# Performance work log

Measured on AMD Instinct MI355X. Metric: run time of the kernel, lower is better.

## Reference

```python
import jax, jax.numpy as jnp
import numpy as np


def setup_inputs() -> dict:
    key = jax.random.key(0)
    k1, k2 = jax.random.split(key)
    pred = jax.random.normal(k1, (16, 4096, 3), dtype=jnp.float32)
    target = jax.random.normal(k2, (16, 4096, 3), dtype=jnp.float32)
    return {"pred": pred, "target": target}


def _pairwise_l2(pc1, pc2):
    # pc1: (B,N,3), pc2: (B,M,3) -> (B,N,M) euclidean distances (torch.cdist p=2)
    sq1 = jnp.sum(pc1 * pc1, axis=-1)  # (B,N)
    sq2 = jnp.sum(pc2 * pc2, axis=-1)  # (B,M)
    inner = jnp.einsum("bnd,bmd->bnm", pc1, pc2)  # (B,N,M)
    d2 = sq1[:, :, None] + sq2[:, None, :] - 2.0 * inner
    return jnp.sqrt(jnp.maximum(d2, 0.0))


def reference(pred, target):
    d = _pairwise_l2(pred, target)          # (B,N,M)
    dist1 = jnp.mean(jnp.min(d, axis=2), axis=1)  # (B,) pred -> target
    dist2 = jnp.mean(jnp.min(d, axis=1), axis=1)  # (B,) target -> pred
    chamfer = (dist1 + dist2) / 2.0         # bidirectional=True
    return jnp.mean(chamfer)
```

## Files before the change

kernel.cpp:

```cpp
#include <hip/hip_runtime.h>
#include <math.h>
#include <stdint.h>


#define BATCH   16
#define NPTS    4096
#define THREADS 256
#define NITEMS  (2 * BATCH * NPTS)
#define MAIN_BLOCKS (2 * BATCH * (NPTS / 128))

typedef __attribute__((ext_vector_type(8)))  _Float16 half8;
typedef __attribute__((ext_vector_type(16))) float    floatx16;

union Pack16 { float4 f4; _Float16 h[8]; half8 h8; };

#define AS1 __attribute__((address_space(1)))
#define AS3 __attribute__((address_space(3)))

__global__ __launch_bounds__(THREADS) void chamfer_prep(
    const float* __restrict__ pred, const float* __restrict__ target,
    float4* __restrict__ packP, float4* __restrict__ packT)
{
    int g = blockIdx.x * THREADS + threadIdx.x;
    int arr = g >> 16;
    int pt  = g & 65535;
    const float* src = arr ? target : pred;
    float x = src[pt * 3 + 0];
    float y = src[pt * 3 + 1];
    float z = src[pt * 3 + 2];
    _Float16 hx = (_Float16)x, hy = (_Float16)y, hz = (_Float16)z;
    float xf = (float)hx, yf = (float)hy, zf = (float)hz;
    float t = xf * xf + yf * yf + zf * zf;
    _Float16 h1 = (_Float16)t;
    _Float16 h2 = (_Float16)(t - (float)h1);
    Pack16 p;
    p.h[0] = hx; p.h[1] = hy; p.h[2] = hz; p.h[3] = h1; p.h[4] = h2;
    p.h[5] = (_Float16)0.0f; p.h[6] = (_Float16)0.0f; p.h[7] = (_Float16)0.0f;
    (arr ? packT : packP)[pt] = p.f4;
}

__global__ __launch_bounds__(THREADS) void chamfer_main(
    const float4* __restrict__ packP, const float4* __restrict__ packT,
    float* __restrict__ blocksum)
{
    __shared__ float4 abuf[128];
    __shared__ float  wsum[4];

    int tid  = threadIdx.x;
    int lane = tid & 63;
    int wave = tid >> 6;
    int l31  = lane & 31;
    bool lo  = lane < 32;

    int id = blockIdx.x;
    int ng = id & 31; id >>= 5;
    int b  = id & 15; id >>= 4;
    int dir = id;

    const float4* qpack = dir ? packT : packP;
    const float4* cpack = dir ? packP : packT;

    Pack16 praw;
    praw.f4 = qpack[(size_t)b * NPTS + ng * 128 + wave * 32 + l31];
    float psq = (float)praw.h[3] + (float)praw.h[4];

    half8 bfrag;
#pragma unroll
    for (int i = 0; i < 8; ++i) bfrag[i] = (_Float16)0.0f;
    if (lo) {
        bfrag[0] = (_Float16)(praw.h[0] * (_Float16)-2.0f);
        bfrag[1] = (_Float16)(praw.h[1] * (_Float16)-2.0f);
        bfrag[2] = (_Float16)(praw.h[2] * (_Float16)-2.0f);
        bfrag[3] = (_Float16)1.0f;
        bfrag[4] = (_Float16)1.0f;
    }

    const float4* cbase = cpack + (size_t)b * NPTS;

    floatx16 zero, mn;
#pragma unroll
    for (int r = 0; r < 16; ++r) { zero[r] = 0.0f; mn[r] = 1e30f; }

    __builtin_amdgcn_global_load_lds(
        (const AS1 uint32_t*)(cbase + lane),
        (AS3 uint32_t*)(&abuf[lane]), 16, 0, 0);

#pragma unroll 2
    for (int t = 0; t < 64; ++t) {
        int cur = (t & 1) * 64;
        if (t < 63) {
            __builtin_amdgcn_global_load_lds(
                (const AS1 uint32_t*)(cbase + (t + 1) * 64 + lane),
                (AS3 uint32_t*)(&abuf[((t + 1) & 1) * 64 + lane]), 16, 0, 0);
            __builtin_amdgcn_s_waitcnt(0x0f71);
        } else {
            __builtin_amdgcn_s_waitcnt(0x0f70);
        }
        Pack16 a0, a1;
        a0.f4 = abuf[cur + l31];
        a1.f4 = abuf[cur + l31 + 32];
        floatx16 d0 = __builtin_amdgcn_mfma_f32_32x32x16_f16(a0.h8, bfrag, zero, 0, 0, 0);
        floatx16 d1 = __builtin_amdgcn_mfma_f32_32x32x16_f16(a1.h8, bfrag, zero, 0, 0, 0);
#pragma unroll
        for (int r = 0; r < 16; ++r)
            mn[r] = fminf(fminf(d0[r], d1[r]), mn[r]);
    }

    float m0 = fminf(fminf(mn[0], mn[1]),  fminf(mn[2], mn[3]));
    float m1 = fminf(fminf(mn[4], mn[5]),  fminf(mn[6], mn[7]));
    float m2 = fminf(fminf(mn[8], mn[9]),  fminf(mn[10], mn[11]));
    float m3 = fminf(fminf(mn[12], mn[13]), fminf(mn[14], mn[15]));
    float m  = fminf(fminf(m0, m1), fminf(m2, m3));
    m = fminf(m, __shfl_xor(m, 32));

    float dist = sqrtf(fmaxf(m + psq, 0.0f));

#pragma unroll
    for (int off = 1; off <= 16; off <<= 1)
        dist += __shfl_xor(dist, off);

    if (lane == 0) wsum[wave] = dist;
    __syncthreads();
    if (tid == 0) blocksum[blockIdx.x] = wsum[0] + wsum[1] + wsum[2] + wsum[3];
}

__global__ __launch_bounds__(THREADS) void chamfer_finish(
    const float4* __restrict__ bs, float* __restrict__ out)
{
    __shared__ float ws[4];
    int tid = threadIdx.x;
    float4 v = bs[tid];
    float s = v.x + v.y + v.z + v.w;
#pragma unroll
    for (int off = 1; off <= 32; off <<= 1)
        s += __shfl_xor(s, off);
    int lane = tid & 63, wave = tid >> 6;
    if (lane == 0) ws[wave] = s;
    __syncthreads();
    if (tid == 0) out[0] = (ws[0] + ws[1] + ws[2] + ws[3]) * (1.0f / (float)NITEMS);
}

extern "C" void kernel_launch(void* const* d_in, const int* in_sizes, int n_in,
                              void* d_out, int out_size, void* d_ws, size_t ws_size,
                              hipStream_t stream) {
    const float* pred   = (const float*)d_in[0];
    const float* target = (const float*)d_in[1];
    float* out = (float*)d_out;

    float4* packP = (float4*)d_ws;
    float4* packT = packP + (size_t)BATCH * NPTS;
    float*  blocksum = (float*)(packT + (size_t)BATCH * NPTS);

    chamfer_prep<<<NITEMS / THREADS, THREADS, 0, stream>>>(pred, target, packP, packT);
    chamfer_main<<<MAIN_BLOCKS, THREADS, 0, stream>>>(packP, packT, blocksum);
    chamfer_finish<<<1, THREADS, 0, stream>>>((const float4*)blocksum, out);
}
```

Measured before the change: 86.49 us.

## Deepen per-wave LDS prefetch ring and fuse final reduction via atomics

The candidate-point prefetch becomes a per-wave 4-slot LDS ring with three loads in flight instead of a shared double buffer, to hide global latency better. The separate finish kernel is removed. Each block atomically adds its partial sum into strided accumulators, and the last block, detected with a counter, reduces them and writes the output. This saves one kernel launch but adds atomic traffic, and makes the fp32 summation order nondeterministic.

Measured after the change: 98.12 us. 1.13x slower.

```diff
diff --git a/kernel.cpp b/kernel.cpp
--- a/kernel.cpp
+++ b/kernel.cpp
@@ -8,6 +8,8 @@
 #define THREADS 256
 #define NITEMS  (2 * BATCH * NPTS)
 #define MAIN_BLOCKS (2 * BATCH * (NPTS / 128))
+#define NACC       64
+#define ACC_STRIDE 16
 
 typedef __attribute__((ext_vector_type(8)))  _Float16 half8;
 typedef __attribute__((ext_vector_type(16))) float    floatx16;
@@ -19,8 +21,14 @@
 
 __global__ __launch_bounds__(THREADS) void chamfer_prep(
     const float* __restrict__ pred, const float* __restrict__ target,
-    float4* __restrict__ packP, float4* __restrict__ packT)
+    float4* __restrict__ packP, float4* __restrict__ packT,
+    float* __restrict__ accum, int* __restrict__ counter)
 {
+    if (blockIdx.x == 0) {
+        if (threadIdx.x < NACC) accum[threadIdx.x * ACC_STRIDE] = 0.0f;
+        if (threadIdx.x == NACC) counter[0] = 0;
+    }
+
     int g = blockIdx.x * THREADS + threadIdx.x;
     int arr = g >> 16;
     int pt  = g & 65535;
@@ -41,10 +49,11 @@
 
 __global__ __launch_bounds__(THREADS) void chamfer_main(
     const float4* __restrict__ packP, const float4* __restrict__ packT,
-    float* __restrict__ blocksum)
+    float* __restrict__ accum, int* __restrict__ counter, float* __restrict__ out)
 {
-    __shared__ float4 abuf[128];
-    __shared__ float  wsum[4];
+    __shared__ __align__(16) float4 abuf[4][4][64];
+    __shared__ float wsum[4];
+    __shared__ int   flag;
 
     int tid  = threadIdx.x;
     int lane = tid & 63;
@@ -81,24 +90,23 @@
 #pragma unroll
     for (int r = 0; r < 16; ++r) { zero[r] = 0.0f; mn[r] = 1e30f; }
 
-    __builtin_amdgcn_global_load_lds(
-        (const AS1 uint32_t*)(cbase + lane),
-        (AS3 uint32_t*)(&abuf[lane]), 16, 0, 0);
+#pragma unroll
+    for (int p = 0; p < 3; ++p)
+        __builtin_amdgcn_global_load_lds(
+            (const AS1 uint32_t*)(cbase + p * 64 + lane),
+            (AS3 uint32_t*)(&abuf[wave][p][lane]), 16, 0, 0);
 
-#pragma unroll 2
+#pragma unroll 4
     for (int t = 0; t < 64; ++t) {
-        int cur = (t & 1) * 64;
-        if (t < 63) {
-            __builtin_amdgcn_global_load_lds(
-                (const AS1 uint32_t*)(cbase + (t + 1) * 64 + lane),
-                (AS3 uint32_t*)(&abuf[((t + 1) & 1) * 64 + lane]), 16, 0, 0);
-            __builtin_amdgcn_s_waitcnt(0x0f71);
-        } else {
-            __builtin_amdgcn_s_waitcnt(0x0f70);
-        }
+        int tn = (t + 3 < 63) ? (t + 3) : 63;
+        __builtin_amdgcn_global_load_lds(
+            (const AS1 uint32_t*)(cbase + tn * 64 + lane),
+            (AS3 uint32_t*)(&abuf[wave][(t + 3) & 3][lane]), 16, 0, 0);
+        __builtin_amdgcn_s_waitcnt(0x0f73);
+
         Pack16 a0, a1;
-        a0.f4 = abuf[cur + l31];
-        a1.f4 = abuf[cur + l31 + 32];
+        a0.f4 = abuf[wave][t & 3][l31];
+        a1.f4 = abuf[wave][t & 3][l31 + 32];
         floatx16 d0 = __builtin_amdgcn_mfma_f32_32x32x16_f16(a0.h8, bfrag, zero, 0, 0, 0);
         floatx16 d1 = __builtin_amdgcn_mfma_f32_32x32x16_f16(a1.h8, bfrag, zero, 0, 0, 0);
 #pragma unroll
@@ -106,9 +114,9 @@
             mn[r] = fminf(fminf(d0[r], d1[r]), mn[r]);
     }
 
-    float m0 = fminf(fminf(mn[0], mn[1]),  fminf(mn[2], mn[3]));
-    float m1 = fminf(fminf(mn[4], mn[5]),  fminf(mn[6], mn[7]));
-    float m2 = fminf(fminf(mn[8], mn[9]),  fminf(mn[10], mn[11]));
+    float m0 = fminf(fminf(mn[0], mn[1]),   fminf(mn[2], mn[3]));
+    float m1 = fminf(fminf(mn[4], mn[5]),   fminf(mn[6], mn[7]));
+    float m2 = fminf(fminf(mn[8], mn[9]),   fminf(mn[10], mn[11]));
     float m3 = fminf(fminf(mn[12], mn[13]), fminf(mn[14], mn[15]));
     float m  = fminf(fminf(m0, m1), fminf(m2, m3));
     m = fminf(m, __shfl_xor(m, 32));
@@ -121,23 +129,23 @@
 
     if (lane == 0) wsum[wave] = dist;
     __syncthreads();
-    if (tid == 0) blocksum[blockIdx.x] = wsum[0] + wsum[1] + wsum[2] + wsum[3];
-}
 
-__global__ __launch_bounds__(THREADS) void chamfer_finish(
-    const float4* __restrict__ bs, float* __restrict__ out)
-{
-    __shared__ float ws[4];
-    int tid = threadIdx.x;
-    float4 v = bs[tid];
-    float s = v.x + v.y + v.z + v.w;
+    if (tid == 0) {
+        float s = wsum[0] + wsum[1] + wsum[2] + wsum[3];
+        atomicAdd(&accum[(blockIdx.x & (NACC - 1)) * ACC_STRIDE], s);
+        __threadfence();
+        int old = atomicAdd(counter, 1);
+        flag = (old == MAIN_BLOCKS - 1) ? 1 : 0;
+    }
+    __syncthreads();
+
+    if (flag && tid < 64) {
+        float v = atomicAdd(&accum[tid * ACC_STRIDE], 0.0f);
 #pragma unroll
-    for (int off = 1; off <= 32; off <<= 1)
-        s += __shfl_xor(s, off);
-    int lane = tid & 63, wave = tid >> 6;
-    if (lane == 0) ws[wave] = s;
-    __syncthreads();
-    if (tid == 0) out[0] = (ws[0] + ws[1] + ws[2] + ws[3]) * (1.0f / (float)NITEMS);
+        for (int off = 1; off <= 32; off <<= 1)
+            v += __shfl_xor(v, off);
+        if (tid == 0) out[0] = v * (1.0f / (float)NITEMS);
+    }
 }
 
 extern "C" void kernel_launch(void* const* d_in, const int* in_sizes, int n_in,
@@ -149,9 +157,11 @@
 
     float4* packP = (float4*)d_ws;
     float4* packT = packP + (size_t)BATCH * NPTS;
-    float*  blocksum = (float*)(packT + (size_t)BATCH * NPTS);
+    float*  accum = (float*)(packT + (size_t)BATCH * NPTS);
+    int*    counter = (int*)(accum + NACC * ACC_STRIDE);
 
-    chamfer_prep<<<NITEMS / THREADS, THREADS, 0, stream>>>(pred, target, packP, packT);
-    chamfer_main<<<MAIN_BLOCKS, THREADS, 0, stream>>>(packP, packT, blocksum);
-    chamfer_finish<<<1, THREADS, 0, stream>>>((const float4*)blocksum, out);
+    chamfer_prep<<<NITEMS / THREADS, THREADS, 0, stream>>>(
+        pred, target, packP, packT, accum, counter);
+    chamfer_main<<<MAIN_BLOCKS, THREADS, 0, stream>>>(
+        packP, packT, accum, counter, out);
 }
```
